# Kernel optimization log

Hardware: AMD Instinct MI355X
Metric: run time of the kernel (lower is better)

Reference implementation:

```python
import jax, jax.numpy as jnp
import numpy as np
from jax import lax

EPS = 1e-6

def build_hh_matrix(V):
    """V: [d, d] rows are (unnormalized) Householder vectors.
    Returns Q = prod_i (I - 2 v_i v_i^T) applied left-to-right, matching
    the torch loop Q <- Q @ (I - 2 v v^T) == Q - 2 (Q v) v^T (rank-1 update)."""
    d = V.shape[0]
    Vn = V / (jnp.linalg.norm(V, axis=1, keepdims=True) + EPS)
    def step(Q, v):
        Qv = Q @ v                      # [d]
        return Q - 2.0 * jnp.outer(Qv, v), None
    Q, _ = lax.scan(step, jnp.eye(d, dtype=V.dtype), Vn)
    return Q


def setup_inputs() -> dict:
    key = jax.random.key(0)
    k1, k2 = jax.random.split(key)
    x = jax.random.normal(k1, (131072, 512), dtype=jnp.float32)
    hd_vecs = jax.random.normal(k2, (1, 512, 512), dtype=jnp.float32)
    return {"x": x, "hd_vecs": hd_vecs}


def reference(x, hd_vecs):
    # n_mat == 1 branch: out = (Q @ x^T)^T = x @ Q^T
    Q = build_hh_matrix(hd_vecs[0])     # [d, d]
    return x @ Q.T                      # [npatches, d]
```

## Files before the change

kernel.cpp:

```cpp
#include <hip/hip_runtime.h>
#include <hip/hip_bf16.h>
#include <stdint.h>

#define EPS 1e-6f

typedef unsigned short ushort_t;
using frag  = __attribute__((ext_vector_type(8))) short;
using f32x4 = __attribute__((ext_vector_type(4))) float;
using fv4   = __attribute__((ext_vector_type(4))) float;

#define SWAITLG() asm volatile("s_waitcnt lgkmcnt(0)" ::: "memory")

__device__ __forceinline__ ushort_t f2bf(float f) {
  uint32_t u = __builtin_bit_cast(uint32_t, f);
  u += 0x7FFFu + ((u >> 16) & 1u);
  return (ushort_t)(u >> 16);
}

__device__ __forceinline__ frag pack8(float4 f0, float4 f1) {
  frag v;
  v[0]=(short)f2bf(f0.x); v[1]=(short)f2bf(f0.y); v[2]=(short)f2bf(f0.z); v[3]=(short)f2bf(f0.w);
  v[4]=(short)f2bf(f1.x); v[5]=(short)f2bf(f1.y); v[6]=(short)f2bf(f1.z); v[7]=(short)f2bf(f1.w);
  return v;
}

__global__ __launch_bounds__(256) void normalize_kernel(const float* __restrict__ V,
                                                        float* __restrict__ Vn) {
  const int gw   = blockIdx.x * 4 + (threadIdx.x >> 6);
  const int lane = threadIdx.x & 63;
  const float4* src = (const float4*)(V + (size_t)gw * 512) + lane * 2;
  float4 a = src[0], c = src[1];
  float s = a.x*a.x + a.y*a.y + a.z*a.z + a.w*a.w
          + c.x*c.x + c.y*c.y + c.z*c.z + c.w*c.w;
  #pragma unroll
  for (int off = 32; off; off >>= 1) s += __shfl_xor(s, off);
  float inv = 1.f / (sqrtf(s) + EPS);
  float4 na = make_float4(a.x*inv, a.y*inv, a.z*inv, a.w*inv);
  float4 nc = make_float4(c.x*inv, c.y*inv, c.z*inv, c.w*inv);
  float4* dst = (float4*)(Vn + (size_t)gw * 512) + lane * 2;
  dst[0] = na; dst[1] = nc;
}

__global__ __launch_bounds__(256) void gram_kernel(const float* __restrict__ Vn,
                                                   float* __restrict__ G) {
  const int gi = blockIdx.x;
  const int b = gi >> 7, i = gi & 127;
  const int w = threadIdx.x >> 6, lane = threadIdx.x & 63;
  const float4* ri = (const float4*)(Vn + (size_t)gi * 512) + lane * 2;
  float4 a0 = ri[0], a1 = ri[1];
  for (int j = i + 1 + w; j < 128; j += 4) {
    const float4* rj = (const float4*)(Vn + (size_t)(b * 128 + j) * 512) + lane * 2;
    float4 c0 = rj[0], c1 = rj[1];
    float s = a0.x*c0.x + a0.y*c0.y + a0.z*c0.z + a0.w*c0.w
            + a1.x*c1.x + a1.y*c1.y + a1.z*c1.z + a1.w*c1.w;
    #pragma unroll
    for (int off = 32; off; off >>= 1) s += __shfl_xor(s, off);
    if (lane == 0) G[(size_t)gi * 128 + j] = s;
  }
}

__global__ __launch_bounds__(256) void trinv_kernel(float* __restrict__ GT) {
  __shared__ float Gs[128][132];
  __shared__ float Ai[64][68];
  __shared__ float Di[64][68];
  __shared__ float C1[64][68];
  const int b = blockIdx.x, tid = threadIdx.x;
  float* Gg = GT + b * 16384;

  {
    const int r = tid >> 1, h = tid & 1;
    const float4* src = (const float4*)(Gg + r * 128 + h * 64);
    float4* dst = (float4*)(&Gs[r][h * 64]);
    #pragma unroll
    for (int e = 0; e < 16; ++e) dst[e] = src[e];
  }
  __syncthreads();

  const int wave = tid >> 6, lane = tid & 63;
  if (wave < 2) {
    const int o = wave * 64;
    float t[64];
    #pragma unroll
    for (int i = 63; i >= 0; --i) {
      float s = (i == lane) ? 1.f : 0.f;
      #pragma unroll
      for (int j = i + 1; j < 64; ++j) s -= Gs[o + i][o + j] * t[j];
      t[i] = 2.f * s;
    }
    float (*OUT)[68] = wave ? Di : Ai;
    #pragma unroll
    for (int i = 0; i < 64; ++i) OUT[i][lane] = t[i];
  }
  __syncthreads();

  const int i0 = (tid >> 4) << 2;
  const int j0 = (tid & 15) << 2;

  {
    fv4 acc[4] = {};
    for (int l = 0; l < 64; l += 4) {
      fv4 g[4], d[4];
      #pragma unroll
      for (int r = 0; r < 4; ++r) g[r] = *(const fv4*)(&Gs[i0 + r][64 + l]);
      #pragma unroll
      for (int r = 0; r < 4; ++r) d[r] = *(const fv4*)(&Di[l + r][j0]);
      #pragma unroll
      for (int r = 0; r < 4; ++r)
        #pragma unroll
        for (int l2 = 0; l2 < 4; ++l2)
          #pragma unroll
          for (int q = 0; q < 4; ++q)
            acc[r][q] = fmaf(g[r][l2], d[l2][q], acc[r][q]);
    }
    #pragma unroll
    for (int r = 0; r < 4; ++r) *(fv4*)(&C1[i0 + r][j0]) = acc[r];
  }
  __syncthreads();

  {
    fv4 acc[4] = {};
    for (int l = 0; l < 64; l += 4) {
      fv4 g[4], d[4];
      #pragma unroll
      for (int r = 0; r < 4; ++r) g[r] = *(const fv4*)(&Ai[i0 + r][l]);
      #pragma unroll
      for (int r = 0; r < 4; ++r) d[r] = *(const fv4*)(&C1[l + r][j0]);
      #pragma unroll
      for (int r = 0; r < 4; ++r)
        #pragma unroll
        for (int l2 = 0; l2 < 4; ++l2)
          #pragma unroll
          for (int q = 0; q < 4; ++q)
            acc[r][q] = fmaf(g[r][l2], d[l2][q], acc[r][q]);
    }
    #pragma unroll
    for (int r = 0; r < 4; ++r)
      #pragma unroll
      for (int q = 0; q < 4; ++q)
        Gg[(64 + j0 + q) * 128 + (i0 + r)] = -acc[r][q];
  }

  {
    const int j = tid >> 1, h = tid & 1;
    if (j < 64) {
      if (h == 0) { for (int i = 0; i < 64; ++i) Gg[j * 128 + i] = Ai[i][j]; }
      else        { for (int i = 0; i < 64; ++i) Gg[j * 128 + 64 + i] = 0.f; }
    } else if (h == 1) {
      for (int i = 0; i < 64; ++i) Gg[j * 128 + 64 + i] = Di[i][j - 64];
    }
  }
}

__global__ __launch_bounds__(256) void chain_kernel(const float* __restrict__ Vn,
                                                    const float* __restrict__ Tt,
                                                    ushort_t* __restrict__ Qf) {
  __shared__ float Qt[4][512];
  __shared__ float Pp[4][4][64];
  __shared__ float Ps[4][128];
  __shared__ float Asm[4][128];
  const int t = threadIdx.x, w = t >> 6, lane = t & 63;
  const int m0 = blockIdx.x * 4;

  for (int idx = t; idx < 2048; idx += 256) {
    int i = idx >> 9, k = idx & 511;
    Qt[i][k] = (m0 + i == k) ? 1.f : 0.f;
  }

  for (int b = 0; b < 4; ++b) {
    if (b == 0) {
      __syncthreads();
      if (t < 128) {
        #pragma unroll
        for (int i = 0; i < 4; ++i) Ps[i][t] = Vn[t * 512 + m0 + i];
      }
      __syncthreads();
    } else {
      for (int ch = 0; ch < 2; ++ch) {
        __syncthreads();
        const int n = ch * 64 + lane;
        const float* vrow = Vn + (size_t)(b * 128 + n) * 512;
        float pa[4] = {0.f, 0.f, 0.f, 0.f};
        #pragma unroll 8
        for (int k4 = 0; k4 < 32; ++k4) {
          int kk = w * 128 + k4 * 4;
          float4 vv = *(const float4*)(vrow + kk);
          #pragma unroll
          for (int i = 0; i < 4; ++i) {
            float4 qq = *(const float4*)(&Qt[i][kk]);
            pa[i] += qq.x*vv.x + qq.y*vv.y + qq.z*vv.z + qq.w*vv.w;
          }
        }
        #pragma unroll
        for (int i = 0; i < 4; ++i) Pp[w][i][lane] = pa[i];
        __syncthreads();
        if (w < 2) {
          #pragma unroll
          for (int i2 = 0; i2 < 2; ++i2) {
            int i = w * 2 + i2;
            Ps[i][ch * 64 + lane] = Pp[0][i][lane] + Pp[1][i][lane]
                                  + Pp[2][i][lane] + Pp[3][i][lane];
          }
        }
      }
      __syncthreads();
    }
    {
      const float* trow = Tt + b * 16384 + (t >> 1) * 128 + (t & 1) * 64;
      float aa[4] = {0.f, 0.f, 0.f, 0.f};
      #pragma unroll 4
      for (int j4 = 0; j4 < 16; ++j4) {
        float4 tv = *(const float4*)(trow + j4 * 4);
        int j = (t & 1) * 64 + j4 * 4;
        #pragma unroll
        for (int i = 0; i < 4; ++i) {
          float4 pv = *(const float4*)(&Ps[i][j]);
          aa[i] += pv.x*tv.x + pv.y*tv.y + pv.z*tv.z + pv.w*tv.w;
        }
      }
      #pragma unroll
      for (int i = 0; i < 4; ++i) {
        float o = __shfl_xor(aa[i], 1);
        if ((t & 1) == 0) Asm[i][t >> 1] = aa[i] + o;
      }
    }
    __syncthreads();
    {
      float acc0[4] = {0.f,0.f,0.f,0.f}, acc1[4] = {0.f,0.f,0.f,0.f};
      const float* vb = Vn + (size_t)b * 65536 + t * 2;
      #pragma unroll 4
      for (int n = 0; n < 128; ++n) {
        float2 vv = *(const float2*)(vb + (size_t)n * 512);
        #pragma unroll
        for (int i = 0; i < 4; ++i) {
          float a = Asm[i][n];
          acc0[i] = fmaf(a, vv.x, acc0[i]);
          acc1[i] = fmaf(a, vv.y, acc1[i]);
        }
      }
      #pragma unroll
      for (int i = 0; i < 4; ++i) {
        Qt[i][t * 2]     -= acc0[i];
        Qt[i][t * 2 + 1] -= acc1[i];
      }
    }
  }
  __syncthreads();
  {
    int i = t >> 6, ks = (t >> 2) & 15, lg = t & 3;
    int r = m0 + i;
    int nt = r >> 4, l = lg * 16 + (r & 15);
    const float* src = &Qt[i][ks * 32 + lg * 8];
    frag v;
    #pragma unroll
    for (int j = 0; j < 8; ++j) v[j] = (short)f2bf(src[j]);
    *(frag*)(Qf + ((size_t)(ks * 32 + nt) * 64 + l) * 8) = v;
  }
}

__global__ __launch_bounds__(512, 3) void final_gemm(const float* __restrict__ X,
                                                     const ushort_t* __restrict__ Qf,
                                                     float* __restrict__ out) {
  __shared__ __align__(16) ushort_t As[2][64 * 64];
  __shared__ __align__(16) float Ep[16][516];
  const int tid = threadIdx.x;
  const int w = tid >> 6, lane = tid & 63;
  const int m0 = blockIdx.x * 64;
  const int row = tid >> 3, seg = tid & 7;
  const int sw_off = row * 128 + ((seg * 16) ^ ((row & 7) << 4));
  const float4* xs = (const float4*)(X + (size_t)(m0 + row) * 512) + seg * 2;

  f32x4 acc[4][4];
  #pragma unroll
  for (int i = 0; i < 4; ++i)
    #pragma unroll
    for (int j = 0; j < 4; ++j) acc[i][j] = (f32x4){0.f, 0.f, 0.f, 0.f};

  float4 fE0 = xs[0], fE1 = xs[1];
  float4 fO0 = xs[16], fO1 = xs[17];
  *(frag*)((char*)As[0] + sw_off) = pack8(fE0, fE1);
  SWAITLG();
  __builtin_amdgcn_s_barrier();

  #pragma unroll
  for (int kt = 0; kt < 8; ++kt) {
    const int cur = kt & 1;
    frag b0[4], b1[4];
    #pragma unroll
    for (int j = 0; j < 4; ++j) {
      int nt = w * 4 + j;
      b0[j] = *(const frag*)(Qf + ((size_t)((2*kt)     * 32 + nt) * 64 + lane) * 8);
      b1[j] = *(const frag*)(Qf + ((size_t)((2*kt + 1) * 32 + nt) * 64 + lane) * 8);
    }
    if (kt < 6) {
      if (cur == 0) { fE0 = xs[(kt + 2) * 16]; fE1 = xs[(kt + 2) * 16 + 1]; }
      else          { fO0 = xs[(kt + 2) * 16]; fO1 = xs[(kt + 2) * 16 + 1]; }
    }
    frag a[4];
    {
      const int kb = (lane >> 4) << 4;
      #pragma unroll
      for (int mf = 0; mf < 4; ++mf) {
        int r = mf * 16 + (lane & 15);
        a[mf] = *(const frag*)((const char*)As[cur] + r * 128 + (kb ^ ((r & 7) << 4)));
      }
      #pragma unroll
      for (int mf = 0; mf < 4; ++mf)
        #pragma unroll
        for (int j = 0; j < 4; ++j)
          acc[mf][j] = __builtin_amdgcn_mfma_f32_16x16x32_bf16(a[mf], b0[j], acc[mf][j], 0, 0, 0);
    }
    {
      const int kb = 64 + ((lane >> 4) << 4);
      #pragma unroll
      for (int mf = 0; mf < 4; ++mf) {
        int r = mf * 16 + (lane & 15);
        a[mf] = *(const frag*)((const char*)As[cur] + r * 128 + (kb ^ ((r & 7) << 4)));
      }
      #pragma unroll
      for (int mf = 0; mf < 4; ++mf)
        #pragma unroll
        for (int j = 0; j < 4; ++j)
          acc[mf][j] = __builtin_amdgcn_mfma_f32_16x16x32_bf16(a[mf], b1[j], acc[mf][j], 0, 0, 0);
    }
    if (kt < 7) {
      float4 c0 = (cur == 0) ? fO0 : fE0;
      float4 c1 = (cur == 0) ? fO1 : fE1;
      *(frag*)((char*)As[cur ^ 1] + sw_off) = pack8(c0, c1);
    }
    SWAITLG();
    __builtin_amdgcn_s_barrier();
  }

  #pragma unroll
  for (int mf = 0; mf < 4; ++mf) {
    if (mf > 0) __builtin_amdgcn_s_barrier();
    #pragma unroll
    for (int j = 0; j < 4; ++j) {
      int col = w * 64 + j * 16 + (lane & 15);
      #pragma unroll
      for (int r = 0; r < 4; ++r)
        Ep[((lane >> 4) << 2) + r][col] = acc[mf][j][r];
    }
    SWAITLG();
    __builtin_amdgcn_s_barrier();
    #pragma unroll
    for (int e = 0; e < 4; ++e) {
      int idx = e * 512 + tid;
      int rr = idx >> 7, c4 = idx & 127;
      float4 v = *(const float4*)(&Ep[rr][c4 * 4]);
      *(float4*)(out + (size_t)(m0 + mf * 16 + rr) * 512 + c4 * 4) = v;
    }
  }
}

extern "C" void kernel_launch(void* const* d_in, const int* in_sizes, int n_in,
                              void* d_out, int out_size, void* d_ws, size_t ws_size,
                              hipStream_t stream) {
  const float* x = (const float*)d_in[0];
  const float* V = (const float*)d_in[1];
  float* out = (float*)d_out;
  float* ws  = (float*)d_ws;

  float*    Vn = ws;
  float*    GT = ws + 262144;
  ushort_t* Qf = (ushort_t*)(ws + 327680);

  normalize_kernel<<<128, 256, 0, stream>>>(V, Vn);
  gram_kernel<<<512, 256, 0, stream>>>(Vn, GT);
  trinv_kernel<<<4, 256, 0, stream>>>(GT);
  chain_kernel<<<128, 256, 0, stream>>>(Vn, GT, Qf);
  final_gemm<<<2048, 512, 0, stream>>>(x, Qf, out);
}
```

Measured before the change: 294.5 us.

## Stream X tiles into LDS via direct global-to-LDS loads with triple buffering

The final GEMM now loads fp32 X tiles straight into LDS with global_load_lds and a three-stage swizzled buffer, converting to bf16 when reading A fragments instead of staging through registers. B fragments are prefetched into a three-slot register ring, so loads overlap the MFMA work. Separately, the chain kernel handles two rows per block across 256 blocks instead of four across 128, to raise parallelism. The cost is more LDS per block (48 KB of fp32 staging), the occupancy hint dropped from the launch bounds, and conversion work repeated in the inner loop.

```diff
diff --git a/kernel.cpp b/kernel.cpp
--- a/kernel.cpp
+++ b/kernel.cpp
@@ -9,18 +9,16 @@
 using f32x4 = __attribute__((ext_vector_type(4))) float;
 using fv4   = __attribute__((ext_vector_type(4))) float;
 
-#define SWAITLG() asm volatile("s_waitcnt lgkmcnt(0)" ::: "memory")
-
 __device__ __forceinline__ ushort_t f2bf(float f) {
   uint32_t u = __builtin_bit_cast(uint32_t, f);
   u += 0x7FFFu + ((u >> 16) & 1u);
   return (ushort_t)(u >> 16);
 }
 
-__device__ __forceinline__ frag pack8(float4 f0, float4 f1) {
+__device__ __forceinline__ frag cvt8(fv4 lo, fv4 hi) {
   frag v;
-  v[0]=(short)f2bf(f0.x); v[1]=(short)f2bf(f0.y); v[2]=(short)f2bf(f0.z); v[3]=(short)f2bf(f0.w);
-  v[4]=(short)f2bf(f1.x); v[5]=(short)f2bf(f1.y); v[6]=(short)f2bf(f1.z); v[7]=(short)f2bf(f1.w);
+  v[0]=(short)f2bf(lo[0]); v[1]=(short)f2bf(lo[1]); v[2]=(short)f2bf(lo[2]); v[3]=(short)f2bf(lo[3]);
+  v[4]=(short)f2bf(hi[0]); v[5]=(short)f2bf(hi[1]); v[6]=(short)f2bf(hi[2]); v[7]=(short)f2bf(hi[3]);
   return v;
 }
 
@@ -154,14 +152,14 @@
 __global__ __launch_bounds__(256) void chain_kernel(const float* __restrict__ Vn,
                                                     const float* __restrict__ Tt,
                                                     ushort_t* __restrict__ Qf) {
-  __shared__ float Qt[4][512];
-  __shared__ float Pp[4][4][64];
-  __shared__ float Ps[4][128];
-  __shared__ float Asm[4][128];
+  __shared__ float Qt[2][512];
+  __shared__ float Pp[4][2][64];
+  __shared__ float Ps[2][128];
+  __shared__ float Asm[2][128];
   const int t = threadIdx.x, w = t >> 6, lane = t & 63;
-  const int m0 = blockIdx.x * 4;
-
-  for (int idx = t; idx < 2048; idx += 256) {
+  const int m0 = blockIdx.x * 2;
+
+  for (int idx = t; idx < 1024; idx += 256) {
     int i = idx >> 9, k = idx & 511;
     Qt[i][k] = (m0 + i == k) ? 1.f : 0.f;
   }
@@ -170,8 +168,8 @@
     if (b == 0) {
       __syncthreads();
       if (t < 128) {
-        #pragma unroll
-        for (int i = 0; i < 4; ++i) Ps[i][t] = Vn[t * 512 + m0 + i];
+        Ps[0][t] = Vn[t * 512 + m0];
+        Ps[1][t] = Vn[t * 512 + m0 + 1];
       }
       __syncthreads();
     } else {
@@ -179,73 +177,68 @@
         __syncthreads();
         const int n = ch * 64 + lane;
         const float* vrow = Vn + (size_t)(b * 128 + n) * 512;
-        float pa[4] = {0.f, 0.f, 0.f, 0.f};
+        float pa[2] = {0.f, 0.f};
         #pragma unroll 8
         for (int k4 = 0; k4 < 32; ++k4) {
           int kk = w * 128 + k4 * 4;
           float4 vv = *(const float4*)(vrow + kk);
           #pragma unroll
-          for (int i = 0; i < 4; ++i) {
+          for (int i = 0; i < 2; ++i) {
             float4 qq = *(const float4*)(&Qt[i][kk]);
             pa[i] += qq.x*vv.x + qq.y*vv.y + qq.z*vv.z + qq.w*vv.w;
           }
         }
         #pragma unroll
-        for (int i = 0; i < 4; ++i) Pp[w][i][lane] = pa[i];
+        for (int i = 0; i < 2; ++i) Pp[w][i][lane] = pa[i];
         __syncthreads();
-        if (w < 2) {
-          #pragma unroll
-          for (int i2 = 0; i2 < 2; ++i2) {
-            int i = w * 2 + i2;
-            Ps[i][ch * 64 + lane] = Pp[0][i][lane] + Pp[1][i][lane]
-                                  + Pp[2][i][lane] + Pp[3][i][lane];
-          }
-        }
+        if (w < 2)
+          Ps[w][ch * 64 + lane] = Pp[0][w][lane] + Pp[1][w][lane]
+                                + Pp[2][w][lane] + Pp[3][w][lane];
       }
       __syncthreads();
     }
     {
       const float* trow = Tt + b * 16384 + (t >> 1) * 128 + (t & 1) * 64;
-      float aa[4] = {0.f, 0.f, 0.f, 0.f};
+      float aa[2] = {0.f, 0.f};
       #pragma unroll 4
       for (int j4 = 0; j4 < 16; ++j4) {
         float4 tv = *(const float4*)(trow + j4 * 4);
         int j = (t & 1) * 64 + j4 * 4;
         #pragma unroll
-        for (int i = 0; i < 4; ++i) {
+        for (int i = 0; i < 2; ++i) {
           float4 pv = *(const float4*)(&Ps[i][j]);
           aa[i] += pv.x*tv.x + pv.y*tv.y + pv.z*tv.z + pv.w*tv.w;
         }
       }
       #pragma unroll
-      for (int i = 0; i < 4; ++i) {
+      for (int i = 0; i < 2; ++i) {
         float o = __shfl_xor(aa[i], 1);
         if ((t & 1) == 0) Asm[i][t >> 1] = aa[i] + o;
       }
     }
     __syncthreads();
     {
-      float acc0[4] = {0.f,0.f,0.f,0.f}, acc1[4] = {0.f,0.f,0.f,0.f};
+      float acc0[2] = {0.f,0.f}, acc1[2] = {0.f,0.f};
       const float* vb = Vn + (size_t)b * 65536 + t * 2;
       #pragma unroll 4
       for (int n = 0; n < 128; ++n) {
         float2 vv = *(const float2*)(vb + (size_t)n * 512);
         #pragma unroll
-        for (int i = 0; i < 4; ++i) {
+        for (int i = 0; i < 2; ++i) {
           float a = Asm[i][n];
           acc0[i] = fmaf(a, vv.x, acc0[i]);
           acc1[i] = fmaf(a, vv.y, acc1[i]);
         }
       }
       #pragma unroll
-      for (int i = 0; i < 4; ++i) {
+      for (int i = 0; i < 2; ++i) {
         Qt[i][t * 2]     -= acc0[i];
         Qt[i][t * 2 + 1] -= acc1[i];
       }
     }
   }
   __syncthreads();
-  {
+  if (t < 128) {
     int i = t >> 6, ks = (t >> 2) & 15, lg = t & 3;
     int r = m0 + i;
     int nt = r >> 4, l = lg * 16 + (r & 15);
@@ -257,17 +250,47 @@
   }
 }
 
-__global__ __launch_bounds__(512, 3) void final_gemm(const float* __restrict__ X,
-                                                     const ushort_t* __restrict__ Qf,
-                                                     float* __restrict__ out) {
-  __shared__ __align__(16) ushort_t As[2][64 * 64];
-  __shared__ __align__(16) float Ep[16][516];
+__global__ __launch_bounds__(512) void final_gemm(const float* __restrict__ X,
+                                                  const ushort_t* __restrict__ Qf,
+                                                  float* __restrict__ out) {
+  __shared__ __align__(16) char smem[49152];
   const int tid = threadIdx.x;
   const int w = tid >> 6, lane = tid & 63;
   const int m0 = blockIdx.x * 64;
-  const int row = tid >> 3, seg = tid & 7;
-  const int sw_off = row * 128 + ((seg * 16) ^ ((row & 7) << 4));
-  const float4* xs = (const float4*)(X + (size_t)(m0 + row) * 512) + seg * 2;
+
+  const int r0 = tid >> 4,          p0 = tid & 15;
+  const int r1 = (tid + 512) >> 4,  p1 = tid & 15;
+  const int g0 = p0 ^ (((r0 & 7) << 1) | ((r0 >> 3) & 1));
+  const int g1 = p1 ^ (((r1 & 7) << 1) | ((r1 >> 3) & 1));
+  const float* src0 = X + (size_t)(m0 + r0) * 512 + g0 * 4;
+  const float* src1 = X + (size_t)(m0 + r1) * 512 + g1 * 4;
+  const int ldsb0 = w * 1024;
+  const int ldsb1 = 8192 + w * 1024;
+
+  #define GLOAD(KT, BUF) do { \
+    __builtin_amdgcn_global_load_lds( \
+      (const __attribute__((address_space(1))) uint32_t*)(src0 + (KT) * 64), \
+      (__attribute__((address_space(3))) uint32_t*)(smem + (BUF) * 16384 + ldsb0), 16, 0, 0); \
+    __builtin_amdgcn_global_load_lds( \
+      (const __attribute__((address_space(1))) uint32_t*)(src1 + (KT) * 64), \
+      (__attribute__((address_space(3))) uint32_t*)(smem + (BUF) * 16384 + ldsb1), 16, 0, 0); \
+  } while (0)
+
+  const ushort_t* qb = Qf + ((size_t)(w * 4) * 64 + lane) * 8;
+  frag bs[3][4];
+  #define BLOAD(KS, SLOT) do { \
+    _Pragma("unroll") \
+    for (int j = 0; j < 4; ++j) \
+      bs[SLOT][j] = *(const frag*)(qb + (size_t)(KS) * 16384 + j * 512); \
+  } while (0)
+
+  int aoff[4];
+  #pragma unroll
+  for (int mf = 0; mf < 4; ++mf) {
+    int row = mf * 16 + (lane & 15);
+    int xm = ((row & 7) << 1) | ((row >> 3) & 1);
+    aoff[mf] = row * 256 + ((((lane >> 4) * 2) ^ xm) << 4);
+  }
 
   f32x4 acc[4][4];
   #pragma unroll
@@ -275,65 +298,52 @@
     #pragma unroll
     for (int j = 0; j < 4; ++j) acc[i][j] = (f32x4){0.f, 0.f, 0.f, 0.f};
 
-  float4 fE0 = xs[0], fE1 = xs[1];
-  float4 fO0 = xs[16], fO1 = xs[17];
-  *(frag*)((char*)As[0] + sw_off) = pack8(fE0, fE1);
-  SWAITLG();
+  GLOAD(0, 0); GLOAD(1, 1); BLOAD(0, 0); BLOAD(1, 1);
+  asm volatile("s_waitcnt vmcnt(10)" ::: "memory");
   __builtin_amdgcn_s_barrier();
 
   #pragma unroll
   for (int kt = 0; kt < 8; ++kt) {
-    const int cur = kt & 1;
-    frag b0[4], b1[4];
-    #pragma unroll
-    for (int j = 0; j < 4; ++j) {
-      int nt = w * 4 + j;
-      b0[j] = *(const frag*)(Qf + ((size_t)((2*kt)     * 32 + nt) * 64 + lane) * 8);
-      b1[j] = *(const frag*)(Qf + ((size_t)((2*kt + 1) * 32 + nt) * 64 + lane) * 8);
-    }
-    if (kt < 6) {
-      if (cur == 0) { fE0 = xs[(kt + 2) * 16]; fE1 = xs[(kt + 2) * 16 + 1]; }
-      else          { fO0 = xs[(kt + 2) * 16]; fO1 = xs[(kt + 2) * 16 + 1]; }
-    }
-    frag a[4];
+    const char* bb = smem + (kt % 3) * 16384;
+    if (kt < 6) GLOAD(kt + 2, (kt + 2) % 3);
+    if (kt < 7) BLOAD(2 * kt + 2, (2 * kt + 2) % 3);
     {
-      const int kb = (lane >> 4) << 4;
+      frag a_[4];
       #pragma unroll
       for (int mf = 0; mf < 4; ++mf) {
-        int r = mf * 16 + (lane & 15);
-        a[mf] = *(const frag*)((const char*)As[cur] + r * 128 + (kb ^ ((r & 7) << 4)));
+        fv4 lo = *(const fv4*)(bb + aoff[mf]);
+        fv4 hi = *(const fv4*)(bb + (aoff[mf] ^ 16));
+        a_[mf] = cvt8(lo, hi);
       }
       #pragma unroll
       for (int mf = 0; mf < 4; ++mf)
         #pragma unroll
         for (int j = 0; j < 4; ++j)
-          acc[mf][j] = __builtin_amdgcn_mfma_f32_16x16x32_bf16(a[mf], b0[j], acc[mf][j], 0, 0, 0);
-    }
+          acc[mf][j] = __builtin_amdgcn_mfma_f32_16x16x32_bf16(a_[mf], bs[(2 * kt) % 3][j], acc[mf][j], 0, 0, 0);
+    }
+    if (kt < 7) BLOAD(2 * kt + 3, (2 * kt + 3) % 3);
     {
-      const int kb = 64 + ((lane >> 4) << 4);
+      frag a_[4];
       #pragma unroll
       for (int mf = 0; mf < 4; ++mf) {
-        int r = mf * 16 + (lane & 15);
-        a[mf] = *(const frag*)((const char*)As[cur] + r * 128 + (kb ^ ((r & 7) << 4)));
+        fv4 lo = *(const fv4*)(bb + (aoff[mf] ^ 128));
+        fv4 hi = *(const fv4*)(bb + (aoff[mf] ^ 128 ^ 16));
+        a_[mf] = cvt8(lo, hi);
       }
       #pragma unroll
       for (int mf = 0; mf < 4; ++mf)
         #pragma unroll
         for (int j = 0; j < 4; ++j)
-          acc[mf][j] = __builtin_amdgcn_mfma_f32_16x16x32_bf16(a[mf], b1[j], acc[mf][j], 0, 0, 0);
-    }
-    if (kt < 7) {
-      float4 c0 = (cur == 0) ? fO0 : fE0;
-      float4 c1 = (cur == 0) ? fO1 : fE1;
-      *(frag*)((char*)As[cur ^ 1] + sw_off) = pack8(c0, c1);
-    }
-    SWAITLG();
+          acc[mf][j] = __builtin_amdgcn_mfma_f32_16x16x32_bf16(a_[mf], bs[(2 * kt + 1) % 3][j], acc[mf][j], 0, 0, 0);
+    }
+    asm volatile("s_waitcnt vmcnt(10)" ::: "memory");
     __builtin_amdgcn_s_barrier();
   }
 
+  float (*Ep)[516] = (float (*)[516])smem;
   #pragma unroll
   for (int mf = 0; mf < 4; ++mf) {
-    if (mf > 0) __builtin_amdgcn_s_barrier();
+    __builtin_amdgcn_s_barrier();
     #pragma unroll
     for (int j = 0; j < 4; ++j) {
       int col = w * 64 + j * 16 + (lane & 15);
@@ -341,7 +351,7 @@
       for (int r = 0; r < 4; ++r)
         Ep[((lane >> 4) << 2) + r][col] = acc[mf][j][r];
     }
-    SWAITLG();
+    asm volatile("s_waitcnt lgkmcnt(0)" ::: "memory");
     __builtin_amdgcn_s_barrier();
     #pragma unroll
     for (int e = 0; e < 4; ++e) {
@@ -351,6 +361,8 @@
       *(float4*)(out + (size_t)(m0 + mf * 16 + rr) * 512 + c4 * 4) = v;
     }
   }
+  #undef GLOAD
+  #undef BLOAD
 }
 
 extern "C" void kernel_launch(void* const* d_in, const int* in_sizes, int n_in,
@@ -368,6 +380,6 @@
   normalize_kernel<<<128, 256, 0, stream>>>(V, Vn);
   gram_kernel<<<512, 256, 0, stream>>>(Vn, GT);
   trinv_kernel<<<4, 256, 0, stream>>>(GT);
-  chain_kernel<<<128, 256, 0, stream>>>(Vn, GT, Qf);
+  chain_kernel<<<256, 256, 0, stream>>>(Vn, GT, Qf);
   final_gemm<<<2048, 512, 0, stream>>>(x, Qf, out);
 }
```

Result: slower. 325.5 us (+10.5%).
